# Kernel optimization log

Measured on AMD Instinct MI355X. Metric: run time of the kernel, lower is better.

Reference implementation:

```python
import jax, jax.numpy as jnp
import numpy as np

THETA = 10000.0
R_TOK = 4  # region_token_num


def _local_positions(regions, max_n):
    # 0-based position of each token within its region (count of prior tokens
    # with the same region id) -- order-based, works for any region layout.
    onehot = jax.nn.one_hot(regions, max_n + 1, dtype=jnp.int32)  # [B,T,N+1]
    counts = jnp.cumsum(onehot, axis=1)                            # inclusive
    return jnp.take_along_axis(counts, regions[..., None], axis=-1)[..., 0] - 1


def _rope(q, k, pos, theta):
    # full-head-dim rotary embedding, split-half convention
    D = q.shape[-1]
    inv_freq = 1.0 / (theta ** (jnp.arange(0, D, 2, dtype=jnp.float32) / D))  # [D/2]
    ang = pos[..., None].astype(jnp.float32) * inv_freq                        # [B,S,D/2]
    cos = jnp.tile(jnp.cos(ang), (1, 1, 2))[:, None]                           # [B,1,S,D]
    sin = jnp.tile(jnp.sin(ang), (1, 1, 2))[:, None]

    def rot(x):
        h = x.shape[-1] // 2
        return jnp.concatenate([-x[..., h:], x[..., :h]], axis=-1)

    return q * cos + rot(q) * sin, k * cos + rot(k) * sin


def setup_inputs() -> dict:
    B, H, D = 2, 16, 64
    T, MAX_N = 2048, 64
    P = MAX_N * R_TOK
    key = jax.random.key(0)
    ks = jax.random.split(key, 7)
    f = lambda k, s: jax.random.normal(k, s, dtype=jnp.float32)
    regions = jnp.sort(jax.random.randint(ks[6], (B, T), 1, MAX_N + 1, dtype=jnp.int32), axis=-1)
    return {
        'pool_q': f(ks[0], (B, H, P, D)),
        'pool_k': f(ks[1], (B, H, P, D)),
        'pool_v': f(ks[2], (B, H, P, D)),
        'x_q': f(ks[3], (B, H, T, D)),
        'x_k': f(ks[4], (B, H, T, D)),
        'x_v': f(ks[5], (B, H, T, D)),
        'regions': regions,
        't_mask': jnp.ones((B, T), dtype=bool),
        'n_mask': jnp.ones((B, MAX_N), dtype=bool),
        'max_n': MAX_N,
    }


def reference(pool_q, pool_k, pool_v, x_q, x_k, x_v, regions, t_mask, n_mask, max_n):
    B, H, P, D = pool_q.shape
    R = R_TOK
    # sequence = [pool, x]
    q = jnp.concatenate([pool_q, x_q], axis=2)
    k = jnp.concatenate([pool_k, x_k], axis=2)
    v = jnp.concatenate([pool_v, x_v], axis=2)

    # local-mode positions (use_pool_offset=False -> pool tokens at pos 0)
    pool_pos = jnp.zeros((B, P), dtype=jnp.int32)
    x_pos = (_local_positions(regions, max_n) + R) * (regions > 0).astype(jnp.int32)
    pos = jnp.concatenate([pool_pos, x_pos], axis=-1)  # [B,S]
    q, k = _rope(q, k, pos, THETA)

    # block-local (same-region) mask: [B,1,S,S], True = allowed
    pool_region = jnp.broadcast_to(jnp.repeat(jnp.arange(1, max_n + 1, dtype=jnp.int32), R)[None], (B, P))
    pool_valid = jnp.repeat(n_mask, R, axis=1)                      # [B,P]
    full_region = jnp.concatenate([pool_region, regions], axis=-1)  # [B,S]
    full_valid = jnp.concatenate([pool_valid, t_mask], axis=-1)     # [B,S]
    same = full_region[:, :, None] == full_region[:, None, :]
    valid = full_valid[:, :, None] & full_valid[:, None, :]
    nonpad = (full_region != 0)[:, :, None] & (full_region != 0)[:, None, :]
    mask = (same & valid & nonpad)[:, None]                          # [B,1,S,S]

    scores = jnp.einsum('bhqd,bhkd->bhqk', q, k) / jnp.sqrt(jnp.float32(D))
    scores = jnp.where(mask, scores, jnp.float32(-1e9))
    attn = jax.nn.softmax(scores, axis=-1)
    out = jnp.einsum('bhqk,bhkd->bhqd', attn, v)
    return out[:, :, :P, :]
```

## Files before the change

kernel.cpp:

```cpp
#include <hip/hip_runtime.h>
#include <hip/hip_bf16.h>

#define BB   2
#define HH   16
#define DD   64
#define TT   2048
#define MAXN 64
#define RTOK 4
#define PP   (MAXN * RTOK)
#define PAD  68

__global__ __launch_bounds__(256)
void build_ranges(const int* __restrict__ regions, int* __restrict__ tab) {
    const int b   = blockIdx.x;
    const int tid = threadIdx.x;
    const int* reg = regions + b * TT;
    int* t = tab + b * 66;
    const int i0 = tid * 8;
    int v[9];
    const int4 a0 = *(const int4*)(reg + i0);
    const int4 a1 = *(const int4*)(reg + i0 + 4);
    v[0] = a0.x; v[1] = a0.y; v[2] = a0.z; v[3] = a0.w;
    v[4] = a1.x; v[5] = a1.y; v[6] = a1.z; v[7] = a1.w;
    v[8] = (tid == 255) ? (MAXN + 1) : reg[i0 + 8];
    if (tid == 0)
        for (int rr = 1; rr <= v[0]; ++rr) t[rr] = 0;
    #pragma unroll
    for (int j = 0; j < 8; ++j)
        for (int rr = v[j] + 1; rr <= v[j + 1]; ++rr) t[rr] = i0 + j + 1;
}

__global__ __launch_bounds__(256, 4)
void lapd_attn(const float* __restrict__ pool_q,
               const float* __restrict__ pool_k,
               const float* __restrict__ pool_v,
               const float* __restrict__ x_k,
               const float* __restrict__ x_v,
               const int* __restrict__ tab,
               float* __restrict__ out) {
    const int blk   = blockIdx.x;
    const int r_idx = blk & (MAXN - 1);
    const int bh    = blk >> 6;
    const int b     = bh / HH;

    const int tid  = threadIdx.x;
    const int wave = tid >> 6;
    const int lane = tid & 63;

    __shared__ float k_s[64][PAD];
    __shared__ float v_t[DD][PAD];
    __shared__ float q_s[4][DD];
    __shared__ float p_s[4][64];

    const size_t poolbase = ((size_t)bh * PP + r_idx * RTOK) * DD;
    const float* pk = pool_k + poolbase;
    const float* pv = pool_v + poolbase;
    const float* xk = x_k + (size_t)bh * TT * DD;
    const float* xv = x_v + (size_t)bh * TT * DD;

    const size_t qidx = poolbase + (size_t)(wave * DD) + lane;
    const float qv = pool_q[qidx] * 0.125f;
    q_s[wave][lane] = qv;

    const int* tb    = tab + b * 66;
    const int start  = tb[r_idx + 1];
    const int cnt    = tb[r_idx + 2] - start;
    const int sstart = (cnt > 0) ? start : 0;

    const int kA = tid >> 3;
    const int d  = (tid & 7) * 4;

    float invf[4];
    #pragma unroll
    for (int c = 0; c < 4; ++c)
        invf[c] = __expf((float)(d + c) * (-9.210340371976184f / 32.0f));

    float acc = 0.0f, l = 0.0f;
    int xbase = 0;
    bool first = true;

    for (;;) {
        const int koff = first ? RTOK : 0;
        int nx = cnt - xbase;
        if (nx > 64 - koff) nx = 64 - koff;
        const int tn = koff + (nx > 0 ? nx : 0);

        float4 klo[2], khi[2], vlo[2], vhi[2];
        int xiv[2];
        bool ispool[2];
        #pragma unroll
        for (int i = 0; i < 2; ++i) {
            const int key = kA + i * 32;
            int xi = key - koff;
            if (xi > nx - 1) xi = nx - 1;
            if (xi < 0) xi = 0;
            xiv[i] = xi;
            ispool[i] = first && (key < RTOK);
            const float* kbase = ispool[i] ? (pk + key * DD)
                               : (xk + (size_t)(sstart + xbase + xi) * DD);
            const float* vbase = ispool[i] ? (pv + key * DD)
                               : (xv + (size_t)(sstart + xbase + xi) * DD);
            klo[i] = *(const float4*)(kbase + d);
            khi[i] = *(const float4*)(kbase + d + 32);
            vlo[i] = *(const float4*)(vbase + d);
            vhi[i] = *(const float4*)(vbase + d + 32);
        }
        #pragma unroll
        for (int i = 0; i < 2; ++i) {
            const int key = kA + i * 32;
            float rlo[4] = {klo[i].x, klo[i].y, klo[i].z, klo[i].w};
            float rhi[4] = {khi[i].x, khi[i].y, khi[i].z, khi[i].w};
            if (!ispool[i]) {
                const float pos = (float)(xbase + xiv[i] + RTOK);
                #pragma unroll
                for (int c = 0; c < 4; ++c) {
                    float sv, cv;
                    __sincosf(pos * invf[c], &sv, &cv);
                    const float lo = rlo[c], hi = rhi[c];
                    rlo[c] = lo * cv - hi * sv;
                    rhi[c] = hi * cv + lo * sv;
                }
            }
            *(float4*)&k_s[key][d]      = make_float4(rlo[0], rlo[1], rlo[2], rlo[3]);
            *(float4*)&k_s[key][d + 32] = make_float4(rhi[0], rhi[1], rhi[2], rhi[3]);
            v_t[d + 0][key] = vlo[i].x;  v_t[d + 32][key] = vhi[i].x;
            v_t[d + 1][key] = vlo[i].y;  v_t[d + 33][key] = vhi[i].y;
            v_t[d + 2][key] = vlo[i].z;  v_t[d + 34][key] = vhi[i].z;
            v_t[d + 3][key] = vlo[i].w;  v_t[d + 35][key] = vhi[i].w;
        }
        __syncthreads();

        float s0 = 0, s1 = 0, s2 = 0, s3 = 0;
        #pragma unroll
        for (int dd2 = 0; dd2 < DD; dd2 += 4) {
            const float4 kk = *(const float4*)&k_s[lane][dd2];
            const float4 qq = *(const float4*)&q_s[wave][dd2];
            s0 += qq.x * kk.x;
            s1 += qq.y * kk.y;
            s2 += qq.z * kk.z;
            s3 += qq.w * kk.w;
        }
        const float s = (s0 + s1) + (s2 + s3);
        p_s[wave][lane] = (lane < tn) ? __expf(s) : 0.0f;

        float a0 = 0, a1 = 0, a2 = 0, a3 = 0, l0 = 0;
        #pragma unroll
        for (int k = 0; k < 64; k += 4) {
            const float4 v4 = *(const float4*)&v_t[lane][k];
            const float p0 = p_s[wave][k + 0];
            const float p1 = p_s[wave][k + 1];
            const float p2 = p_s[wave][k + 2];
            const float p3 = p_s[wave][k + 3];
            a0 += p0 * v4.x;
            a1 += p1 * v4.y;
            a2 += p2 * v4.z;
            a3 += p3 * v4.w;
            l0 += (p0 + p1) + (p2 + p3);
        }
        acc += (a0 + a1) + (a2 + a3);
        l   += l0;

        xbase += (nx > 0 ? nx : 0);
        first = false;
        if (xbase >= cnt) break;
        __syncthreads();
    }

    out[qidx] = acc / l;
}

extern "C" void kernel_launch(void* const* d_in, const int* in_sizes, int n_in,
                              void* d_out, int out_size, void* d_ws, size_t ws_size,
                              hipStream_t stream) {
    const float* pool_q  = (const float*)d_in[0];
    const float* pool_k  = (const float*)d_in[1];
    const float* pool_v  = (const float*)d_in[2];
    const float* x_k     = (const float*)d_in[4];
    const float* x_v     = (const float*)d_in[5];
    const int*   regions = (const int*)d_in[6];
    float*       out     = (float*)d_out;
    int*         tab     = (int*)d_ws;

    build_ranges<<<dim3(BB), dim3(256), 0, stream>>>(regions, tab);
    lapd_attn<<<dim3(BB * HH * MAXN), dim3(256), 0, stream>>>(
        pool_q, pool_k, pool_v, x_k, x_v, tab, out);
}
```

Measured before the change: 115.1 us.

## Compute QK scores with bf16 MFMA directly from registers, drop K shared staging

Replaces the shared-memory K tile and scalar QK dot product with a 16x16x32 bf16 MFMA. Each wave loads its own 16 keys, applies RoPE in registers and converts Q and K to bf16. The V transpose is reorganised so each thread writes float2 pairs to shared memory. This removes the k_s and q_s buffers and the per-lane 64-step dot loop, at the cost of bf16 rounding in the scores and more sincos work per thread (8 per key instead of 4).

```diff
diff --git a/kernel.cpp b/kernel.cpp
--- a/kernel.cpp
+++ b/kernel.cpp
@@ -9,6 +9,15 @@
 #define RTOK 4
 #define PP   (MAXN * RTOK)
 #define PAD  68
+
+typedef short v8s __attribute__((ext_vector_type(8)));
+typedef float v4f __attribute__((ext_vector_type(4)));
+
+__device__ __forceinline__ unsigned short f2bf(float f) {
+    unsigned u = __float_as_uint(f);
+    u += 0x7FFFu + ((u >> 16) & 1u);
+    return (unsigned short)(u >> 16);
+}
 
 __global__ __launch_bounds__(256)
 void build_ranges(const int* __restrict__ regions, int* __restrict__ tab) {
@@ -47,10 +56,13 @@
     const int wave = tid >> 6;
     const int lane = tid & 63;
 
-    __shared__ float k_s[64][PAD];
     __shared__ float v_t[DD][PAD];
-    __shared__ float q_s[4][DD];
     __shared__ float p_s[4][64];
+
+    const int* tb    = tab + b * 66;
+    const int start  = tb[r_idx + 1];
+    const int cnt    = tb[r_idx + 2] - start;
+    const int sstart = (cnt > 0) ? start : 0;
 
     const size_t poolbase = ((size_t)bh * PP + r_idx * RTOK) * DD;
     const float* pk = pool_k + poolbase;
@@ -58,23 +70,35 @@
     const float* xk = x_k + (size_t)bh * TT * DD;
     const float* xv = x_v + (size_t)bh * TT * DD;
 
+    const int quad = lane >> 4;
+    const int j0   = quad * 8;
+    v8s aq0, aq1;
+    {
+        const float* qrow = pool_q + poolbase + (size_t)((lane & 3) * DD);
+        const float4 f0 = *(const float4*)(qrow + j0);
+        const float4 f1 = *(const float4*)(qrow + j0 + 4);
+        const float4 f2 = *(const float4*)(qrow + j0 + 32);
+        const float4 f3 = *(const float4*)(qrow + j0 + 36);
+        const float lo[8] = {f0.x, f0.y, f0.z, f0.w, f1.x, f1.y, f1.z, f1.w};
+        const float hi[8] = {f2.x, f2.y, f2.z, f2.w, f3.x, f3.y, f3.z, f3.w};
+        #pragma unroll
+        for (int c = 0; c < 8; ++c) {
+            aq0[c] = (short)f2bf(lo[c] * 0.125f);
+            aq1[c] = (short)f2bf(hi[c] * 0.125f);
+        }
+    }
+
+    float invf[8];
+    #pragma unroll
+    for (int c = 0; c < 8; ++c)
+        invf[c] = __expf((float)(j0 + c) * (-9.210340371976184f / 32.0f));
+
+    const int keyloc = lane & 15;
+    const int key    = wave * 16 + keyloc;
+    const int vg = tid & 31;
+    const int vc = tid >> 5;
+
     const size_t qidx = poolbase + (size_t)(wave * DD) + lane;
-    const float qv = pool_q[qidx] * 0.125f;
-    q_s[wave][lane] = qv;
-
-    const int* tb    = tab + b * 66;
-    const int start  = tb[r_idx + 1];
-    const int cnt    = tb[r_idx + 2] - start;
-    const int sstart = (cnt > 0) ? start : 0;
-
-    const int kA = tid >> 3;
-    const int d  = (tid & 7) * 4;
-
-    float invf[4];
-    #pragma unroll
-    for (int c = 0; c < 4; ++c)
-        invf[c] = __expf((float)(d + c) * (-9.210340371976184f / 32.0f));
-
     float acc = 0.0f, l = 0.0f;
     int xbase = 0;
     bool first = true;
@@ -83,84 +107,90 @@
         const int koff = first ? RTOK : 0;
         int nx = cnt - xbase;
         if (nx > 64 - koff) nx = 64 - koff;
-        const int tn = koff + (nx > 0 ? nx : 0);
-
-        float4 klo[2], khi[2], vlo[2], vhi[2];
-        int xiv[2];
-        bool ispool[2];
+        if (nx < 0) nx = 0;
+        const int tn = koff + nx;
+
+        int xi = key - koff;
+        if (xi > nx - 1) xi = nx - 1;
+        if (xi < 0) xi = 0;
+        const bool ispool = first && (key < RTOK);
+        const float* kb = ispool ? (pk + key * DD)
+                                 : (xk + (size_t)(sstart + xbase + xi) * DD);
+        const float4 k0 = *(const float4*)(kb + j0);
+        const float4 k1 = *(const float4*)(kb + j0 + 4);
+        const float4 k2 = *(const float4*)(kb + j0 + 32);
+        const float4 k3 = *(const float4*)(kb + j0 + 36);
+
+        float4 vb[2][2];
         #pragma unroll
         for (int i = 0; i < 2; ++i) {
-            const int key = kA + i * 32;
-            int xi = key - koff;
-            if (xi > nx - 1) xi = nx - 1;
-            if (xi < 0) xi = 0;
-            xiv[i] = xi;
-            ispool[i] = first && (key < RTOK);
-            const float* kbase = ispool[i] ? (pk + key * DD)
-                               : (xk + (size_t)(sstart + xbase + xi) * DD);
-            const float* vbase = ispool[i] ? (pv + key * DD)
-                               : (xv + (size_t)(sstart + xbase + xi) * DD);
-            klo[i] = *(const float4*)(kbase + d);
-            khi[i] = *(const float4*)(kbase + d + 32);
-            vlo[i] = *(const float4*)(vbase + d);
-            vhi[i] = *(const float4*)(vbase + d + 32);
-        }
-        #pragma unroll
-        for (int i = 0; i < 2; ++i) {
-            const int key = kA + i * 32;
-            float rlo[4] = {klo[i].x, klo[i].y, klo[i].z, klo[i].w};
-            float rhi[4] = {khi[i].x, khi[i].y, khi[i].z, khi[i].w};
-            if (!ispool[i]) {
-                const float pos = (float)(xbase + xiv[i] + RTOK);
-                #pragma unroll
-                for (int c = 0; c < 4; ++c) {
-                    float sv, cv;
-                    __sincosf(pos * invf[c], &sv, &cv);
-                    const float lo = rlo[c], hi = rhi[c];
-                    rlo[c] = lo * cv - hi * sv;
-                    rhi[c] = hi * cv + lo * sv;
-                }
+            const int vkey = 2 * vg + i;
+            int vxi = vkey - koff;
+            if (vxi > nx - 1) vxi = nx - 1;
+            if (vxi < 0) vxi = 0;
+            const bool vpool = first && (vkey < RTOK);
+            const float* vbp = vpool ? (pv + vkey * DD)
+                                     : (xv + (size_t)(sstart + xbase + vxi) * DD);
+            vb[i][0] = *(const float4*)(vbp + 8 * vc);
+            vb[i][1] = *(const float4*)(vbp + 8 * vc + 4);
+        }
+
+        float klo[8] = {k0.x, k0.y, k0.z, k0.w, k1.x, k1.y, k1.z, k1.w};
+        float khi[8] = {k2.x, k2.y, k2.z, k2.w, k3.x, k3.y, k3.z, k3.w};
+        if (!ispool) {
+            const float pos = (float)(xbase + xi + RTOK);
+            #pragma unroll
+            for (int c = 0; c < 8; ++c) {
+                float sv, cv;
+                __sincosf(pos * invf[c], &sv, &cv);
+                const float lo = klo[c], hi = khi[c];
+                klo[c] = lo * cv - hi * sv;
+                khi[c] = hi * cv + lo * sv;
             }
-            *(float4*)&k_s[key][d]      = make_float4(rlo[0], rlo[1], rlo[2], rlo[3]);
-            *(float4*)&k_s[key][d + 32] = make_float4(rhi[0], rhi[1], rhi[2], rhi[3]);
-            v_t[d + 0][key] = vlo[i].x;  v_t[d + 32][key] = vhi[i].x;
-            v_t[d + 1][key] = vlo[i].y;  v_t[d + 33][key] = vhi[i].y;
-            v_t[d + 2][key] = vlo[i].z;  v_t[d + 34][key] = vhi[i].z;
-            v_t[d + 3][key] = vlo[i].w;  v_t[d + 35][key] = vhi[i].w;
-        }
+        }
+        v8s bk0, bk1;
+        #pragma unroll
+        for (int c = 0; c < 8; ++c) {
+            bk0[c] = (short)f2bf(klo[c]);
+            bk1[c] = (short)f2bf(khi[c]);
+        }
+
+        v4f cs = {0.0f, 0.0f, 0.0f, 0.0f};
+        cs = __builtin_amdgcn_mfma_f32_16x16x32_bf16(aq0, bk0, cs, 0, 0, 0);
+        cs = __builtin_amdgcn_mfma_f32_16x16x32_bf16(aq1, bk1, cs, 0, 0, 0);
+        if (quad == 0) {
+            #pragma unroll
+            for (int r2 = 0; r2 < 4; ++r2)
+                p_s[r2][key] = (key < tn) ? __expf(cs[r2]) : 0.0f;
+        }
+
+        #pragma unroll
+        for (int mh = 0; mh < 2; ++mh)
+            #pragma unroll
+            for (int c = 0; c < 4; ++c) {
+                const int d = 8 * vc + 4 * mh + c;
+                *(float2*)&v_t[d][2 * vg] =
+                    make_float2(((const float*)&vb[0][mh])[c],
+                                ((const float*)&vb[1][mh])[c]);
+            }
+
         __syncthreads();
-
-        float s0 = 0, s1 = 0, s2 = 0, s3 = 0;
-        #pragma unroll
-        for (int dd2 = 0; dd2 < DD; dd2 += 4) {
-            const float4 kk = *(const float4*)&k_s[lane][dd2];
-            const float4 qq = *(const float4*)&q_s[wave][dd2];
-            s0 += qq.x * kk.x;
-            s1 += qq.y * kk.y;
-            s2 += qq.z * kk.z;
-            s3 += qq.w * kk.w;
-        }
-        const float s = (s0 + s1) + (s2 + s3);
-        p_s[wave][lane] = (lane < tn) ? __expf(s) : 0.0f;
 
         float a0 = 0, a1 = 0, a2 = 0, a3 = 0, l0 = 0;
         #pragma unroll
         for (int k = 0; k < 64; k += 4) {
             const float4 v4 = *(const float4*)&v_t[lane][k];
-            const float p0 = p_s[wave][k + 0];
-            const float p1 = p_s[wave][k + 1];
-            const float p2 = p_s[wave][k + 2];
-            const float p3 = p_s[wave][k + 3];
-            a0 += p0 * v4.x;
-            a1 += p1 * v4.y;
-            a2 += p2 * v4.z;
-            a3 += p3 * v4.w;
-            l0 += (p0 + p1) + (p2 + p3);
+            const float4 p4 = *(const float4*)&p_s[wave][k];
+            a0 += p4.x * v4.x;
+            a1 += p4.y * v4.y;
+            a2 += p4.z * v4.z;
+            a3 += p4.w * v4.w;
+            l0 += (p4.x + p4.y) + (p4.z + p4.w);
         }
         acc += (a0 + a1) + (a2 + a3);
         l   += l0;
 
-        xbase += (nx > 0 ? nx : 0);
+        xbase += nx;
         first = false;
         if (xbase >= cnt) break;
         __syncthreads();
```

Measured after the change: 123.0 us. 6.9% more time.
